# Optimization experiments

Hardware: AMD Instinct MI355X
Metric: run time of the kernel (lower is better)

## Reference

```python
import jax, jax.numpy as jnp
import numpy as np

NUM_HEADS = 16
NUM_KV_HEADS = 8
HEAD_DIM = 128
EPS = 1e-6
SLIDING_WINDOW = 1024
ROPE_THETA = 10000.0


def _rms_norm(x, w):
    # per-head RMSNorm in fp32, as in Qwen3RMSNorm
    xf = x.astype(jnp.float32)
    var = jnp.mean(xf * xf, axis=-1, keepdims=True)
    return (w * (xf * jax.lax.rsqrt(var + EPS))).astype(x.dtype)


def _rotate_half(x):
    d = x.shape[-1] // 2
    return jnp.concatenate([-x[..., d:], x[..., :d]], axis=-1)


def setup_inputs() -> dict:
    key = jax.random.key(0)
    ks = jax.random.split(key, 6)
    B, S, H = 2, 2048, 2048
    hidden_states = jax.random.normal(ks[0], (B, S, H), dtype=jnp.float32)
    # RoPE tables per HF convention: cos/sin of shape [B, S, head_dim]
    inv_freq = 1.0 / (ROPE_THETA ** (np.arange(0, HEAD_DIM, 2, dtype=np.float32) / HEAD_DIM))
    pos = np.arange(S, dtype=np.float32)
    ang = np.outer(pos, inv_freq)  # [S, HEAD_DIM/2]
    emb = np.concatenate([ang, ang], axis=-1)  # [S, HEAD_DIM]
    cos = jnp.broadcast_to(jnp.asarray(np.cos(emb)), (B, S, HEAD_DIM))
    sin = jnp.broadcast_to(jnp.asarray(np.sin(emb)), (B, S, HEAD_DIM))
    sc = 0.02
    Wq = jax.random.normal(ks[1], (NUM_HEADS * HEAD_DIM, H), dtype=jnp.float32) * sc
    Wk = jax.random.normal(ks[2], (NUM_KV_HEADS * HEAD_DIM, H), dtype=jnp.float32) * sc
    Wv = jax.random.normal(ks[3], (NUM_KV_HEADS * HEAD_DIM, H), dtype=jnp.float32) * sc
    Wo = jax.random.normal(ks[4], (H, NUM_HEADS * HEAD_DIM), dtype=jnp.float32) * sc
    q_norm_w = jnp.ones((HEAD_DIM,), dtype=jnp.float32)
    k_norm_w = jnp.ones((HEAD_DIM,), dtype=jnp.float32)
    return {"hidden_states": hidden_states, "cos": cos, "sin": sin,
            "Wq": Wq, "Wk": Wk, "Wv": Wv, "Wo": Wo,
            "q_norm_w": q_norm_w, "k_norm_w": k_norm_w}


def reference(hidden_states, cos, sin, Wq, Wk, Wv, Wo, q_norm_w, k_norm_w):
    B, S, H = hidden_states.shape
    scaling = HEAD_DIM ** -0.5
    # projections (torch Linear: y = x @ W.T), reshape to [B, nH, S, D]
    q = jnp.einsum('bsh,oh->bso', hidden_states, Wq).reshape(B, S, NUM_HEADS, HEAD_DIM)
    k = jnp.einsum('bsh,oh->bso', hidden_states, Wk).reshape(B, S, NUM_KV_HEADS, HEAD_DIM)
    v = jnp.einsum('bsh,oh->bso', hidden_states, Wv).reshape(B, S, NUM_KV_HEADS, HEAD_DIM)
    q = _rms_norm(q, q_norm_w).transpose(0, 2, 1, 3)  # [B, nH, S, D]
    k = _rms_norm(k, k_norm_w).transpose(0, 2, 1, 3)  # [B, nKV, S, D]
    v = v.transpose(0, 2, 1, 3)
    # RoPE, cos/sin broadcast over heads (unsqueeze_dim=1)
    c = cos[:, None, :, :]
    s = sin[:, None, :, :]
    q = q * c + _rotate_half(q) * s
    k = k * c + _rotate_half(k) * s
    # GQA: repeat kv heads
    groups = NUM_HEADS // NUM_KV_HEADS
    k = jnp.repeat(k, groups, axis=1)
    v = jnp.repeat(v, groups, axis=1)
    # causal + sliding-window mask
    i = jnp.arange(S)[:, None]
    j = jnp.arange(S)[None, :]
    mask = (j <= i) & (i - j < SLIDING_WINDOW)  # [S, S]
    scores = jnp.einsum('bhqd,bhkd->bhqk', q, k) * scaling
    scores = jnp.where(mask[None, None], scores, jnp.finfo(scores.dtype).min)
    probs = jax.nn.softmax(scores, axis=-1)
    attn = jnp.einsum('bhqk,bhkd->bhqd', probs, v)  # [B, nH, S, D]
    attn = attn.transpose(0, 2, 1, 3).reshape(B, S, NUM_HEADS * HEAD_DIM)
    out = jnp.einsum('bso,ho->bsh', attn, Wo)
    return out
```

## Files before the change

kernel.cpp:

```cpp
#include <hip/hip_runtime.h>
#include <stdint.h>

#define S_LEN 2048
#define BATCH 2
#define HID 2048
#define NH 16
#define NKV 8
#define HD 128
#define WINDOW 1024
#define SCALE 0.08838834764831845f
#define QKVW 4096

typedef unsigned short u16;
typedef unsigned int u32;
typedef __attribute__((ext_vector_type(8))) short short8;
typedef __attribute__((ext_vector_type(4))) float f32x4;
typedef __attribute__((ext_vector_type(16))) float f32x16;
typedef __attribute__((ext_vector_type(4))) u16 u16x4;

__device__ __forceinline__ u16 f2b(float f) {
  u32 u = __builtin_bit_cast(u32, f);
  return (u16)((u + 0x7fffu + ((u >> 16) & 1u)) >> 16);
}
__device__ __forceinline__ float b2f(u16 h) {
  u32 u = ((u32)h) << 16;
  return __builtin_bit_cast(float, u);
}
__device__ __forceinline__ u32 pk_bf16(float a, float b) {
  u32 d;
  asm("v_cvt_pk_bf16_f32 %0, %1, %2" : "=v"(d) : "v"(a), "v"(b));
  return d;
}

__device__ __forceinline__ void gload_lds16(const u16* g, u16* l) {
  __builtin_amdgcn_global_load_lds(
      (const __attribute__((address_space(1))) u32*)g,
      (__attribute__((address_space(3))) u32*)l, 16, 0, 0);
}

template <int N>
__device__ __forceinline__ void wait_vm() {
  if constexpr (N == 0) asm volatile("s_waitcnt vmcnt(0)" ::: "memory");
}

#define CQ0 2097152
#define CQ1 3145728
#define CQ2 3670016
#define CQ3 4194304
#define CQ4 5242880
__global__ __launch_bounds__(256) void k_conv5(const float* __restrict__ s0,
                                               const float* __restrict__ s1,
                                               const float* __restrict__ s2,
                                               const float* __restrict__ s3,
                                               const float* __restrict__ s4,
                                               u16* __restrict__ dst) {
  int i = blockIdx.x * blockDim.x + threadIdx.x;
  const int st = gridDim.x * blockDim.x;
  for (; i < CQ4; i += st) {
    const f32x4* src;
    if (i < CQ0)      src = (const f32x4*)s0 + i;
    else if (i < CQ1) src = (const f32x4*)s1 + (i - CQ0);
    else if (i < CQ2) src = (const f32x4*)s2 + (i - CQ1);
    else if (i < CQ3) src = (const f32x4*)s3 + (i - CQ2);
    else              src = (const f32x4*)s4 + (i - CQ3);
    f32x4 v = *src;
    u16x4 o;
    o[0] = f2b(v[0]); o[1] = f2b(v[1]); o[2] = f2b(v[2]); o[3] = f2b(v[3]);
    ((u16x4*)dst)[i] = o;
  }
}

__device__ __forceinline__ void store_c(u16* C, long idx, float v) { C[idx] = f2b(v); }
__device__ __forceinline__ void store_c(float* C, long idx, float v) { C[idx] = v; }

template <typename OutT>
__global__ __launch_bounds__(256, 4) void k_gemmS(const u16* __restrict__ A,
                                                  const u16* __restrict__ B,
                                                  OutT* __restrict__ C,
                                                  int M, int N, int K) {
  __shared__ u16 sA[128 * 64];
  __shared__ u16 sB[128 * 64];
  const int tid = threadIdx.x;
  const int lane = tid & 63;
  const int w = tid >> 6;
  const int l15 = lane & 15;
  const int lg = lane >> 4;
  const int wm = w >> 1;
  const int wn = w & 1;
  const int sw = l15 & 7;

  const int gx = gridDim.x;
  const int nwg = gx * gridDim.y;
  const int flat = blockIdx.y * gx + blockIdx.x;
  const int tile = (flat & 7) * (nwg >> 3) + (flat >> 3);
  const long m0 = (long)(tile / gx) * 128;
  const long n0 = (long)(tile % gx) * 128;

  const u16* Abase = A + m0 * K;
  const u16* Bbase = B + n0 * K;

  int aOff[4], bOff[4], dstOff[4];
#pragma unroll
  for (int i = 0; i < 4; ++i) {
    const int c = tid + i * 256;
    const int row = c >> 3, chs = c & 7;
    const int scol = (chs ^ (row & 7)) * 8;
    aOff[i] = row * K + scol;
    bOff[i] = row * K + scol;
    dstOff[i] = c * 8;
  }

  f32x4 acc[4][4];
  const f32x4 z4 = {0.f, 0.f, 0.f, 0.f};
#pragma unroll
  for (int i = 0; i < 4; ++i)
#pragma unroll
    for (int j = 0; j < 4; ++j) acc[i][j] = z4;

  const int arow = (wm * 64 + l15) * 64;
  const int brow = (wn * 64 + l15) * 64;
  const int akc0 = (lg ^ sw) * 8;
  const int akc1 = ((4 + lg) ^ sw) * 8;

  const int NT = K >> 6;

  for (int t = 0; t < NT; ++t) {
#pragma unroll
    for (int i = 0; i < 4; ++i)
      gload_lds16(Abase + aOff[i] + t * 64, &sA[dstOff[i]]);
#pragma unroll
    for (int i = 0; i < 4; ++i)
      gload_lds16(Bbase + bOff[i] + t * 64, &sB[dstOff[i]]);
    wait_vm<0>();
    __builtin_amdgcn_sched_barrier(0);
    __builtin_amdgcn_s_barrier();
    __builtin_amdgcn_sched_barrier(0);

#pragma unroll
    for (int kk = 0; kk < 2; ++kk) {
      const int akc = (kk == 0) ? akc0 : akc1;
      short8 afk[4], bfk[4];
#pragma unroll
      for (int i = 0; i < 4; ++i)
        afk[i] = *(const short8*)&sA[arow + i * 16 * 64 + akc];
#pragma unroll
      for (int j = 0; j < 4; ++j)
        bfk[j] = *(const short8*)&sB[brow + j * 16 * 64 + akc];
      __builtin_amdgcn_s_setprio(1);
#pragma unroll
      for (int i = 0; i < 4; ++i)
#pragma unroll
        for (int j = 0; j < 4; ++j)
          acc[i][j] = __builtin_amdgcn_mfma_f32_16x16x32_bf16(
              afk[i], bfk[j], acc[i][j], 0, 0, 0);
      __builtin_amdgcn_s_setprio(0);
    }
    __builtin_amdgcn_s_barrier();
    __builtin_amdgcn_sched_barrier(0);
  }

#pragma unroll
  for (int i = 0; i < 4; ++i)
#pragma unroll
    for (int j = 0; j < 4; ++j)
#pragma unroll
      for (int r = 0; r < 4; ++r) {
        long row = m0 + wm * 64 + i * 16 + lg * 4 + r;
        long col = n0 + wn * 64 + j * 16 + l15;
        store_c(C, row * (long)N + col, acc[i][j][r]);
      }
}

__global__ __launch_bounds__(256) void k_normrope(u16* __restrict__ QKV,
                                                  const float* __restrict__ cosb,
                                                  const float* __restrict__ sinb,
                                                  const float* __restrict__ qw,
                                                  const float* __restrict__ kw) {
  const int lane = threadIdx.x & 63;
  const int w = threadIdx.x >> 6;
  int row = blockIdx.x * 4 + w;
  const int nQ = BATCH * S_LEN * NH;
  u16* p;
  const float* nw;
  int tok;
  float sc;
  if (row < nQ) {
    tok = row >> 4;
    int h = row & 15;
    p = QKV + (long)tok * QKVW + h * HD;
    nw = qw;
    sc = SCALE;
  } else {
    int r2 = row - nQ;
    tok = r2 >> 3;
    int h = r2 & 7;
    p = QKV + (long)tok * QKVW + 2048 + h * HD;
    nw = kw;
    sc = 1.0f;
  }
  float x0 = b2f(p[lane]);
  float x1 = b2f(p[lane + 64]);
  float ss = x0 * x0 + x1 * x1;
#pragma unroll
  for (int mk = 1; mk < 64; mk <<= 1) ss += __shfl_xor(ss, mk, 64);
  float rinv = rsqrtf(ss * (1.0f / 128.0f) + 1e-6f);
  float y0 = x0 * rinv * nw[lane];
  float y1 = x1 * rinv * nw[lane + 64];
  const float* cp = cosb + (long)tok * HD;
  const float* sp = sinb + (long)tok * HD;
  float o0 = (y0 * cp[lane] - y1 * sp[lane]) * sc;
  float o1 = (y1 * cp[lane + 64] + y0 * sp[lane + 64]) * sc;
  p[lane] = f2b(o0);
  p[lane + 64] = f2b(o1);
}

__global__ __launch_bounds__(256, 2) void k_attn(const u16* __restrict__ QKV,
                                                 u16* __restrict__ AO) {
  __shared__ u16 sK[64 * 128];
  __shared__ u16 sVT[64 * 128];
  const int tid = threadIdx.x;
  const int lane = tid & 63;
  const int l31 = lane & 31;
  const int hi = lane >> 5;
  const int w = tid >> 6;
  const int q0 = blockIdx.x * 128;
  const int h = blockIdx.y;
  const int b = blockIdx.z;
  const int kvh = h >> 1;
  const int qw0 = q0 + w * 32;
  const int iq = qw0 + l31;

  const long tokbase = (long)b * S_LEN;
  const u16* Qrow = QKV + (tokbase + qw0 + l31) * QKVW + h * HD;
  short8 qf[8];
#pragma unroll
  for (int dt = 0; dt < 8; ++dt) qf[dt] = *(const short8*)(Qrow + dt * 16 + hi * 8);

  f32x16 o[4];
#pragma unroll
  for (int n = 0; n < 4; ++n)
#pragma unroll
    for (int r = 0; r < 16; ++r) o[n][r] = 0.f;
  float m = 0.f, lsum = 0.f;

  const u16* Kbase = QKV + tokbase * QKVW + 2048 + kvh * HD;
  const u16* Vbase = QKV + tokbase * QKVW + 3072 + kvh * HD;

  int kc_row[4], kc_off[4];
  u16* kc_dst[4];
#pragma unroll
  for (int i = 0; i < 4; ++i) {
    const int c = tid + 256 * i;
    kc_row[i] = c >> 4;
    kc_off[i] = (((c & 15) ^ ((c >> 4) & 7))) * 8;
    kc_dst[i] = &sK[c * 8];
  }
  const int rp = tid & 31;
  const int dc0 = tid >> 5;
  const int rg_st = rp >> 2;

  int t_lo = q0 - (WINDOW - 1);
  t_lo = (t_lo < 0 ? 0 : t_lo) >> 6;
  const int t_hi = (q0 + 127) >> 6;

  for (int t = t_lo; t <= t_hi; ++t) {
    const int kv0 = t << 6;
#pragma unroll
    for (int i = 0; i < 4; ++i)
      gload_lds16(Kbase + (long)(kv0 + kc_row[i]) * QKVW + kc_off[i], kc_dst[i]);
#pragma unroll
    for (int i = 0; i < 2; ++i) {
      const int dc = dc0 + i * 8;
      const u16* vp = Vbase + (long)(kv0 + 2 * rp) * QKVW + dc * 8;
      short8 v0 = *(const short8*)vp;
      short8 v1 = *(const short8*)(vp + QKVW);
#pragma unroll
      for (int e = 0; e < 8; ++e) {
        const int d = dc * 8 + e;
        const int unit = d * 8 + (rg_st ^ (d & 7));
        ((u32*)sVT)[unit * 4 + (rp & 3)] = (u32)(u16)v0[e] | ((u32)(u16)v1[e] << 16);
      }
    }
    __syncthreads();

    const bool skipw = (kv0 > qw0 + 31) || (kv0 + 63 < qw0 - (WINDOW - 1));
    if (!skipw) {
      const bool full = (kv0 + 63 <= qw0) && ((qw0 + 31) - kv0 < WINDOW);
      f32x16 s0, s1;
#pragma unroll
      for (int r = 0; r < 16; ++r) { s0[r] = 0.f; s1[r] = 0.f; }
      const int rsw = l31 & 7;
#pragma unroll
      for (int dt = 0; dt < 8; ++dt) {
        const int ch = hi + 2 * dt;
        const short8 kf0 = *(const short8*)&sK[(l31 * 16 + (ch ^ rsw)) * 8];
        s0 = __builtin_amdgcn_mfma_f32_32x32x16_bf16(kf0, qf[dt], s0, 0, 0, 0);
        const short8 kf1 = *(const short8*)&sK[((l31 + 32) * 16 + (ch ^ rsw)) * 8];
        s1 = __builtin_amdgcn_mfma_f32_32x32x16_bf16(kf1, qf[dt], s1, 0, 0, 0);
      }
      float p[32];
#pragma unroll
      for (int r = 0; r < 16; ++r) { p[r] = s0[r]; p[16 + r] = s1[r]; }
      if (!full) {
#pragma unroll
        for (int r = 0; r < 32; ++r) {
          const int kk = kv0 + (r >> 4) * 32 + 4 * hi + (r & 3) + 8 * ((r >> 2) & 3);
          p[r] = ((u32)(iq - kk) < (u32)WINDOW) ? p[r] : -3.0e38f;
        }
      }
      float tm = p[0];
#pragma unroll
      for (int r = 1; r < 32; ++r) tm = fmaxf(tm, p[r]);
      tm = fmaxf(tm, __shfl_xor(tm, 32, 64));
      const float mn = fmaxf(m, tm);
      const float al = __expf(m - mn);
      m = mn;
      float rs = 0.f;
#pragma unroll
      for (int r = 0; r < 32; ++r) { p[r] = __expf(p[r] - mn); rs += p[r]; }
      rs += __shfl_xor(rs, 32, 64);
      lsum = lsum * al + rs;
#pragma unroll
      for (int n = 0; n < 4; ++n)
#pragma unroll
        for (int r = 0; r < 16; ++r) o[n][r] *= al;

      short8 pf[4];
#pragma unroll
      for (int ks = 0; ks < 4; ++ks) {
        const int bb = (ks >> 1) * 16 + (ks & 1) * 8;
        u32 a0 = pk_bf16(p[bb + 0], p[bb + 1]);
        u32 b0 = pk_bf16(p[bb + 4], p[bb + 5]);
        u32 a1 = pk_bf16(p[bb + 2], p[bb + 3]);
        u32 b1 = pk_bf16(p[bb + 6], p[bb + 7]);
        asm volatile("v_permlane32_swap_b32 %0, %1" : "+v"(a0), "+v"(b0));
        asm volatile("v_permlane32_swap_b32 %0, %1" : "+v"(a1), "+v"(b1));
        union { u32 u[4]; short8 s; } uu;
        uu.u[0] = a0; uu.u[1] = a1; uu.u[2] = b0; uu.u[3] = b1;
        pf[ks] = uu.s;
      }
#pragma unroll
      for (int dt = 0; dt < 4; ++dt) {
        const int d = l31 + 32 * dt;
        const int dsw = d & 7;
#pragma unroll
        for (int ks = 0; ks < 4; ++ks) {
          const int rg = ks * 2 + hi;
          const short8 vf = *(const short8*)&sVT[(d * 8 + (rg ^ dsw)) * 8];
          o[dt] = __builtin_amdgcn_mfma_f32_32x32x16_bf16(vf, pf[ks], o[dt], 0, 0, 0);
        }
      }
    }
    __syncthreads();
  }

  __syncthreads();
  float* R = ((float*)sK) + w * 1024;
  const float rl = 1.0f / lsum;
  const int half = hi;
#pragma unroll
  for (int dt = 0; dt < 4; ++dt) {
#pragma unroll
    for (int r = 0; r < 16; ++r) {
      const int dp = 4 * hi + (r & 3) + 8 * (r >> 2);
      R[dp * 32 + (l31 ^ (4 * (dp & 7)))] = o[dt][r] * rl;
    }
    __syncthreads();
    union { u16 hh[16]; short8 s[2]; } U;
#pragma unroll
    for (int j = 0; j < 16; ++j) {
      const int dp = half * 16 + j;
      U.hh[j] = f2b(R[dp * 32 + (l31 ^ (4 * (dp & 7)))]);
    }
    u16* dst = AO + (tokbase + q0 + w * 32 + l31) * (NH * HD) + h * HD + dt * 32 + half * 16;
    *(short8*)dst = U.s[0];
    *(short8*)(dst + 8) = U.s[1];
    __syncthreads();
  }
}

extern "C" void kernel_launch(void* const* d_in, const int* in_sizes, int n_in,
                              void* d_out, int out_size, void* d_ws, size_t ws_size,
                              hipStream_t stream) {
  const float* hs   = (const float*)d_in[0];
  const float* cosb = (const float*)d_in[1];
  const float* sinb = (const float*)d_in[2];
  const float* Wq   = (const float*)d_in[3];
  const float* Wk   = (const float*)d_in[4];
  const float* Wv   = (const float*)d_in[5];
  const float* Wo   = (const float*)d_in[6];
  const float* qw   = (const float*)d_in[7];
  const float* kw   = (const float*)d_in[8];
  float* out = (float*)d_out;

  const long SZ_X  = (long)BATCH * S_LEN * HID;
  const long SZ_WQ = (long)NH * HD * HID;
  const long SZ_WK = (long)NKV * HD * HID;
  u16* Xb   = (u16*)d_ws;
  u16* Wqb  = Xb + SZ_X;
  u16* Wkb  = Wqb + SZ_WQ;
  u16* Wvb  = Wkb + SZ_WK;
  u16* Wob  = Wvb + SZ_WK;
  u16* QKVb = Wob + SZ_WQ;
  u16* AOb  = QKVb + (long)BATCH * S_LEN * QKVW;

  k_conv5<<<2048, 256, 0, stream>>>(hs, Wq, Wk, Wv, Wo, Xb);

  k_gemmS<u16><<<dim3(32, 32), 256, 0, stream>>>(
      Xb, Wqb, QKVb, BATCH * S_LEN, QKVW, HID);

  k_normrope<<<(BATCH * S_LEN * (NH + NKV)) / 4, 256, 0, stream>>>(QKVb, cosb, sinb, qw, kw);

  k_attn<<<dim3(S_LEN / 128, NH, BATCH), 256, 0, stream>>>(QKVb, AOb);

  k_gemmS<float><<<dim3(16, 32), 256, 0, stream>>>(
      AOb, Wob, out, BATCH * S_LEN, HID, HID);
}
```

Baseline: 209.0 us.

## Use 2-wave 128x128 GEMM variant with larger per-wave tiles for QKV projection

Adds a k_gemmV kernel that computes the same 128x128 output tile with 128 threads (2 waves) instead of 256, each wave covering all 128 rows by 64 columns with an 8x4 MFMA accumulator grid. The QKV projection GEMM launch switches to this kernel. The aim is more MFMA work per LDS fragment load and fewer waves sharing each barrier. In exchange, register pressure roughly doubles and occupancy drops (launch bounds of 2 blocks), with fewer waves available to hide load latency. The shared A/B offset array in k_gemmS is a minor cleanup.

```diff
diff --git a/kernel.cpp b/kernel.cpp
--- a/kernel.cpp
+++ b/kernel.cpp
@@ -74,6 +74,99 @@
 __device__ __forceinline__ void store_c(float* C, long idx, float v) { C[idx] = v; }
 
 template <typename OutT>
+__global__ __launch_bounds__(128, 2) void k_gemmV(const u16* __restrict__ A,
+                                                  const u16* __restrict__ B,
+                                                  OutT* __restrict__ C,
+                                                  int M, int N, int K) {
+  __shared__ u16 sA[128 * 64];
+  __shared__ u16 sB[128 * 64];
+  const int tid = threadIdx.x;
+  const int lane = tid & 63;
+  const int w = tid >> 6;
+  const int l15 = lane & 15;
+  const int lg = lane >> 4;
+  const int sw = l15 & 7;
+
+  const int gx = gridDim.x;
+  const int nwg = gx * gridDim.y;
+  const int flat = blockIdx.y * gx + blockIdx.x;
+  const int tile = (flat & 7) * (nwg >> 3) + (flat >> 3);
+  const long m0 = (long)(tile / gx) * 128;
+  const long n0 = (long)(tile % gx) * 128;
+
+  const u16* Abase = A + m0 * K;
+  const u16* Bbase = B + n0 * K;
+
+  int aOff[8], dstOff[8];
+#pragma unroll
+  for (int i = 0; i < 8; ++i) {
+    const int c = tid + i * 128;
+    const int row = c >> 3, chs = c & 7;
+    aOff[i] = row * K + (chs ^ (row & 7)) * 8;
+    dstOff[i] = c * 8;
+  }
+
+  f32x4 acc[8][4];
+  const f32x4 z4 = {0.f, 0.f, 0.f, 0.f};
+#pragma unroll
+  for (int i = 0; i < 8; ++i)
+#pragma unroll
+    for (int j = 0; j < 4; ++j) acc[i][j] = z4;
+
+  const int akc0 = (lg ^ sw) * 8;
+  const int akc1 = ((4 + lg) ^ sw) * 8;
+  const int brow0 = w * 64;
+
+  const int NT = K >> 6;
+
+  for (int t = 0; t < NT; ++t) {
+#pragma unroll
+    for (int i = 0; i < 8; ++i)
+      gload_lds16(Abase + aOff[i] + t * 64, &sA[dstOff[i]]);
+#pragma unroll
+    for (int i = 0; i < 8; ++i)
+      gload_lds16(Bbase + aOff[i] + t * 64, &sB[dstOff[i]]);
+    wait_vm<0>();
+    __builtin_amdgcn_sched_barrier(0);
+    __builtin_amdgcn_s_barrier();
+    __builtin_amdgcn_sched_barrier(0);
+
+#pragma unroll
+    for (int kk = 0; kk < 2; ++kk) {
+      const int akc = (kk == 0) ? akc0 : akc1;
+      short8 afk[8], bfk[4];
+#pragma unroll
+      for (int i = 0; i < 8; ++i)
+        afk[i] = *(const short8*)&sA[(i * 16 + l15) * 64 + akc];
+#pragma unroll
+      for (int j = 0; j < 4; ++j)
+        bfk[j] = *(const short8*)&sB[(brow0 + j * 16 + l15) * 64 + akc];
+      __builtin_amdgcn_s_setprio(1);
+#pragma unroll
+      for (int i = 0; i < 8; ++i)
+#pragma unroll
+        for (int j = 0; j < 4; ++j)
+          acc[i][j] = __builtin_amdgcn_mfma_f32_16x16x32_bf16(
+              afk[i], bfk[j], acc[i][j], 0, 0, 0);
+      __builtin_amdgcn_s_setprio(0);
+    }
+    __builtin_amdgcn_s_barrier();
+    __builtin_amdgcn_sched_barrier(0);
+  }
+
+#pragma unroll
+  for (int i = 0; i < 8; ++i)
+#pragma unroll
+    for (int j = 0; j < 4; ++j)
+#pragma unroll
+      for (int r = 0; r < 4; ++r) {
+        long row = m0 + i * 16 + lg * 4 + r;
+        long col = n0 + w * 64 + j * 16 + l15;
+        store_c(C, row * (long)N + col, acc[i][j][r]);
+      }
+}
+
+template <typename OutT>
 __global__ __launch_bounds__(256, 4) void k_gemmS(const u16* __restrict__ A,
                                                   const u16* __restrict__ B,
                                                   OutT* __restrict__ C,
@@ -99,14 +192,12 @@
   const u16* Abase = A + m0 * K;
   const u16* Bbase = B + n0 * K;
 
-  int aOff[4], bOff[4], dstOff[4];
+  int aOff[4], dstOff[4];
 #pragma unroll
   for (int i = 0; i < 4; ++i) {
     const int c = tid + i * 256;
     const int row = c >> 3, chs = c & 7;
-    const int scol = (chs ^ (row & 7)) * 8;
-    aOff[i] = row * K + scol;
-    bOff[i] = row * K + scol;
+    aOff[i] = row * K + (chs ^ (row & 7)) * 8;
     dstOff[i] = c * 8;
   }
 
@@ -130,7 +221,7 @@
       gload_lds16(Abase + aOff[i] + t * 64, &sA[dstOff[i]]);
 #pragma unroll
     for (int i = 0; i < 4; ++i)
-      gload_lds16(Bbase + bOff[i] + t * 64, &sB[dstOff[i]]);
+      gload_lds16(Bbase + aOff[i] + t * 64, &sB[dstOff[i]]);
     wait_vm<0>();
     __builtin_amdgcn_sched_barrier(0);
     __builtin_amdgcn_s_barrier();
@@ -406,7 +497,7 @@
 
   k_conv5<<<2048, 256, 0, stream>>>(hs, Wq, Wk, Wv, Wo, Xb);
 
-  k_gemmS<u16><<<dim3(32, 32), 256, 0, stream>>>(
+  k_gemmV<u16><<<dim3(32, 32), 128, 0, stream>>>(
       Xb, Wqb, QKVb, BATCH * S_LEN, QKVW, HID);
 
   k_normrope<<<(BATCH * S_LEN * (NH + NKV)) / 4, 256, 0, stream>>>(QKVb, cosb, sinb, qw, kw);
```

Result: faster. 203.2 us (-2.8%).

## Fuse Q norm and RoPE into attention, add lazy softmax rescale

Applied to the files above, without the earlier changes.

Q-side RMSNorm, RoPE and scaling now run inside the attention kernel on the loaded Q fragments, so the separate norm kernel handles only K heads. This removes a read and write pass over Q. The online softmax now skips the max update and rescaling of the output accumulators unless the new tile max exceeds the running max by more than 8. The GEMM launch-bounds occupancy hint rises from 4 to 5, and the duplicate B offset array is dropped. The lazy rescale risks larger intermediate values, and the tighter register budget may cause spills in the GEMM.

```diff
diff --git a/kernel.cpp b/kernel.cpp
--- a/kernel.cpp
+++ b/kernel.cpp
@@ -74,7 +74,7 @@
 __device__ __forceinline__ void store_c(float* C, long idx, float v) { C[idx] = v; }
 
 template <typename OutT>
-__global__ __launch_bounds__(256, 4) void k_gemmS(const u16* __restrict__ A,
+__global__ __launch_bounds__(256, 5) void k_gemmS(const u16* __restrict__ A,
                                                   const u16* __restrict__ B,
                                                   OutT* __restrict__ C,
                                                   int M, int N, int K) {
@@ -99,14 +99,12 @@
   const u16* Abase = A + m0 * K;
   const u16* Bbase = B + n0 * K;
 
-  int aOff[4], bOff[4], dstOff[4];
+  int aOff[4], dstOff[4];
 #pragma unroll
   for (int i = 0; i < 4; ++i) {
     const int c = tid + i * 256;
     const int row = c >> 3, chs = c & 7;
-    const int scol = (chs ^ (row & 7)) * 8;
-    aOff[i] = row * K + scol;
-    bOff[i] = row * K + scol;
+    aOff[i] = row * K + (chs ^ (row & 7)) * 8;
     dstOff[i] = c * 8;
   }
 
@@ -130,7 +128,7 @@
       gload_lds16(Abase + aOff[i] + t * 64, &sA[dstOff[i]]);
 #pragma unroll
     for (int i = 0; i < 4; ++i)
-      gload_lds16(Bbase + bOff[i] + t * 64, &sB[dstOff[i]]);
+      gload_lds16(Bbase + aOff[i] + t * 64, &sB[dstOff[i]]);
     wait_vm<0>();
     __builtin_amdgcn_sched_barrier(0);
     __builtin_amdgcn_s_barrier();
@@ -171,51 +169,35 @@
       }
 }
 
-__global__ __launch_bounds__(256) void k_normrope(u16* __restrict__ QKV,
-                                                  const float* __restrict__ cosb,
-                                                  const float* __restrict__ sinb,
-                                                  const float* __restrict__ qw,
-                                                  const float* __restrict__ kw) {
+__global__ __launch_bounds__(256) void k_normropeK(u16* __restrict__ QKV,
+                                                   const float* __restrict__ cosb,
+                                                   const float* __restrict__ sinb,
+                                                   const float* __restrict__ kw) {
   const int lane = threadIdx.x & 63;
   const int w = threadIdx.x >> 6;
-  int row = blockIdx.x * 4 + w;
-  const int nQ = BATCH * S_LEN * NH;
-  u16* p;
-  const float* nw;
-  int tok;
-  float sc;
-  if (row < nQ) {
-    tok = row >> 4;
-    int h = row & 15;
-    p = QKV + (long)tok * QKVW + h * HD;
-    nw = qw;
-    sc = SCALE;
-  } else {
-    int r2 = row - nQ;
-    tok = r2 >> 3;
-    int h = r2 & 7;
-    p = QKV + (long)tok * QKVW + 2048 + h * HD;
-    nw = kw;
-    sc = 1.0f;
-  }
+  const int row = blockIdx.x * 4 + w;
+  const int tok = row >> 3;
+  const int h = row & 7;
+  u16* p = QKV + (long)tok * QKVW + 2048 + h * HD;
   float x0 = b2f(p[lane]);
   float x1 = b2f(p[lane + 64]);
   float ss = x0 * x0 + x1 * x1;
 #pragma unroll
   for (int mk = 1; mk < 64; mk <<= 1) ss += __shfl_xor(ss, mk, 64);
   float rinv = rsqrtf(ss * (1.0f / 128.0f) + 1e-6f);
-  float y0 = x0 * rinv * nw[lane];
-  float y1 = x1 * rinv * nw[lane + 64];
+  float y0 = x0 * rinv * kw[lane];
+  float y1 = x1 * rinv * kw[lane + 64];
   const float* cp = cosb + (long)tok * HD;
   const float* sp = sinb + (long)tok * HD;
-  float o0 = (y0 * cp[lane] - y1 * sp[lane]) * sc;
-  float o1 = (y1 * cp[lane + 64] + y0 * sp[lane + 64]) * sc;
-  p[lane] = f2b(o0);
-  p[lane + 64] = f2b(o1);
+  p[lane] = f2b(y0 * cp[lane] - y1 * sp[lane]);
+  p[lane + 64] = f2b(y1 * cp[lane + 64] + y0 * sp[lane + 64]);
 }
 
 __global__ __launch_bounds__(256, 2) void k_attn(const u16* __restrict__ QKV,
-                                                 u16* __restrict__ AO) {
+                                                 u16* __restrict__ AO,
+                                                 const float* __restrict__ qwp,
+                                                 const float* __restrict__ cosb,
+                                                 const float* __restrict__ sinb) {
   __shared__ u16 sK[64 * 128];
   __shared__ u16 sVT[64 * 128];
   const int tid = threadIdx.x;
@@ -231,10 +213,39 @@
   const int iq = qw0 + l31;
 
   const long tokbase = (long)b * S_LEN;
-  const u16* Qrow = QKV + (tokbase + qw0 + l31) * QKVW + h * HD;
+  const long gtok = tokbase + qw0 + l31;
+  const u16* Qrow = QKV + gtok * QKVW + h * HD;
   short8 qf[8];
 #pragma unroll
   for (int dt = 0; dt < 8; ++dt) qf[dt] = *(const short8*)(Qrow + dt * 16 + hi * 8);
+  {
+    float ss = 0.f;
+#pragma unroll
+    for (int dt = 0; dt < 8; ++dt)
+#pragma unroll
+      for (int j = 0; j < 8; ++j) {
+        const float f = b2f((u16)qf[dt][j]);
+        ss += f * f;
+      }
+    ss += __shfl_xor(ss, 32, 64);
+    const float rinv = rsqrtf(ss * (1.0f / 128.0f) + 1e-6f);
+    const float* cp = cosb + gtok * HD;
+    const float* sp = sinb + gtok * HD;
+#pragma unroll
+    for (int dt = 0; dt < 4; ++dt) {
+      const int d0 = dt * 16 + hi * 8;
+#pragma unroll
+      for (int j = 0; j < 8; ++j) {
+        const int d = d0 + j;
+        const float y0 = b2f((u16)qf[dt][j]) * rinv * qwp[d];
+        const float y1 = b2f((u16)qf[dt + 4][j]) * rinv * qwp[d + 64];
+        const float o0 = (y0 * cp[d] - y1 * sp[d]) * SCALE;
+        const float o1 = (y1 * cp[d + 64] + y0 * sp[d + 64]) * SCALE;
+        qf[dt][j] = (short)f2b(o0);
+        qf[dt + 4][j] = (short)f2b(o1);
+      }
+    }
+  }
 
   f32x16 o[4];
 #pragma unroll
@@ -312,18 +323,21 @@
 #pragma unroll
       for (int r = 1; r < 32; ++r) tm = fmaxf(tm, p[r]);
       tm = fmaxf(tm, __shfl_xor(tm, 32, 64));
-      const float mn = fmaxf(m, tm);
-      const float al = __expf(m - mn);
-      m = mn;
+      if (!__all(tm - m <= 8.0f)) {
+        const float mn = fmaxf(m, tm);
+        const float al = __expf(m - mn);
+        m = mn;
+        lsum *= al;
+#pragma unroll
+        for (int n = 0; n < 4; ++n)
+#pragma unroll
+          for (int r = 0; r < 16; ++r) o[n][r] *= al;
+      }
       float rs = 0.f;
 #pragma unroll
-      for (int r = 0; r < 32; ++r) { p[r] = __expf(p[r] - mn); rs += p[r]; }
+      for (int r = 0; r < 32; ++r) { p[r] = __expf(p[r] - m); rs += p[r]; }
       rs += __shfl_xor(rs, 32, 64);
-      lsum = lsum * al + rs;
-#pragma unroll
-      for (int n = 0; n < 4; ++n)
-#pragma unroll
-        for (int r = 0; r < 16; ++r) o[n][r] *= al;
+      lsum += rs;
 
       short8 pf[4];
 #pragma unroll
@@ -409,9 +423,9 @@
   k_gemmS<u16><<<dim3(32, 32), 256, 0, stream>>>(
       Xb, Wqb, QKVb, BATCH * S_LEN, QKVW, HID);
 
-  k_normrope<<<(BATCH * S_LEN * (NH + NKV)) / 4, 256, 0, stream>>>(QKVb, cosb, sinb, qw, kw);
-
-  k_attn<<<dim3(S_LEN / 128, NH, BATCH), 256, 0, stream>>>(QKVb, AOb);
+  k_normropeK<<<(BATCH * S_LEN * NKV) / 4, 256, 0, stream>>>(QKVb, cosb, sinb, kw);
+
+  k_attn<<<dim3(S_LEN / 128, NH, BATCH), 256, 0, stream>>>(QKVb, AOb, qw, cosb, sinb);
 
   k_gemmS<float><<<dim3(16, 32), 256, 0, stream>>>(
       AOb, Wob, out, BATCH * S_LEN, HID, HID);
```

Measured after the change: 473.0 us. +126.3%, slower.

## Share K/V tiles across GQA head pair in one 512-thread attention block

Applied to the files above, without the earlier changes.

The attention kernel now launches one 512-thread block per KV head instead of one 256-thread block per query head. Both query heads of a GQA group use the same K and V tiles staged in LDS, which halves global K/V loads and LDS staging work per query head. It also adds a lazy online-softmax rescale: the running max and the output accumulators are rescaled only when some lane's new max exceeds the old by more than 8. Larger blocks can lower occupancy and raise barrier cost, and skipping the rescale lets exponentials reach up to e^8 before normalization.

```diff
diff --git a/kernel.cpp b/kernel.cpp
--- a/kernel.cpp
+++ b/kernel.cpp
@@ -99,14 +99,12 @@
   const u16* Abase = A + m0 * K;
   const u16* Bbase = B + n0 * K;
 
-  int aOff[4], bOff[4], dstOff[4];
+  int aOff[4], dstOff[4];
 #pragma unroll
   for (int i = 0; i < 4; ++i) {
     const int c = tid + i * 256;
     const int row = c >> 3, chs = c & 7;
-    const int scol = (chs ^ (row & 7)) * 8;
-    aOff[i] = row * K + scol;
-    bOff[i] = row * K + scol;
+    aOff[i] = row * K + (chs ^ (row & 7)) * 8;
     dstOff[i] = c * 8;
   }
 
@@ -130,7 +128,7 @@
       gload_lds16(Abase + aOff[i] + t * 64, &sA[dstOff[i]]);
 #pragma unroll
     for (int i = 0; i < 4; ++i)
-      gload_lds16(Bbase + bOff[i] + t * 64, &sB[dstOff[i]]);
+      gload_lds16(Bbase + aOff[i] + t * 64, &sB[dstOff[i]]);
     wait_vm<0>();
     __builtin_amdgcn_sched_barrier(0);
     __builtin_amdgcn_s_barrier();
@@ -214,20 +212,21 @@
   p[lane + 64] = f2b(o1);
 }
 
-__global__ __launch_bounds__(256, 2) void k_attn(const u16* __restrict__ QKV,
+__global__ __launch_bounds__(512, 2) void k_attn(const u16* __restrict__ QKV,
                                                  u16* __restrict__ AO) {
-  __shared__ u16 sK[64 * 128];
-  __shared__ u16 sVT[64 * 128];
+  __shared__ u16 smem[2 * 64 * 128];
+  u16* const sK = smem;
+  u16* const sVT = smem + 64 * 128;
   const int tid = threadIdx.x;
   const int lane = tid & 63;
   const int l31 = lane & 31;
   const int hi = lane >> 5;
   const int w = tid >> 6;
   const int q0 = blockIdx.x * 128;
-  const int h = blockIdx.y;
+  const int kvh = blockIdx.y;
   const int b = blockIdx.z;
-  const int kvh = h >> 1;
-  const int qw0 = q0 + w * 32;
+  const int h = kvh * 2 + (w >> 2);
+  const int qw0 = q0 + (w & 3) * 32;
   const int iq = qw0 + l31;
 
   const long tokbase = (long)b * S_LEN;
@@ -246,17 +245,17 @@
   const u16* Kbase = QKV + tokbase * QKVW + 2048 + kvh * HD;
   const u16* Vbase = QKV + tokbase * QKVW + 3072 + kvh * HD;
 
-  int kc_row[4], kc_off[4];
-  u16* kc_dst[4];
-#pragma unroll
-  for (int i = 0; i < 4; ++i) {
-    const int c = tid + 256 * i;
+  int kc_row[2], kc_off[2];
+  u16* kc_dst[2];
+#pragma unroll
+  for (int i = 0; i < 2; ++i) {
+    const int c = tid + 512 * i;
     kc_row[i] = c >> 4;
     kc_off[i] = (((c & 15) ^ ((c >> 4) & 7))) * 8;
     kc_dst[i] = &sK[c * 8];
   }
   const int rp = tid & 31;
-  const int dc0 = tid >> 5;
+  const int dc = tid >> 5;
   const int rg_st = rp >> 2;
 
   int t_lo = q0 - (WINDOW - 1);
@@ -266,11 +265,9 @@
   for (int t = t_lo; t <= t_hi; ++t) {
     const int kv0 = t << 6;
 #pragma unroll
-    for (int i = 0; i < 4; ++i)
+    for (int i = 0; i < 2; ++i)
       gload_lds16(Kbase + (long)(kv0 + kc_row[i]) * QKVW + kc_off[i], kc_dst[i]);
-#pragma unroll
-    for (int i = 0; i < 2; ++i) {
-      const int dc = dc0 + i * 8;
+    {
       const u16* vp = Vbase + (long)(kv0 + 2 * rp) * QKVW + dc * 8;
       short8 v0 = *(const short8*)vp;
       short8 v1 = *(const short8*)(vp + QKVW);
@@ -312,18 +309,21 @@
 #pragma unroll
       for (int r = 1; r < 32; ++r) tm = fmaxf(tm, p[r]);
       tm = fmaxf(tm, __shfl_xor(tm, 32, 64));
-      const float mn = fmaxf(m, tm);
-      const float al = __expf(m - mn);
-      m = mn;
+      if (!__all(tm - m <= 8.0f)) {
+        const float mn = fmaxf(m, tm);
+        const float al = __expf(m - mn);
+        m = mn;
+        lsum *= al;
+#pragma unroll
+        for (int n = 0; n < 4; ++n)
+#pragma unroll
+          for (int r = 0; r < 16; ++r) o[n][r] *= al;
+      }
       float rs = 0.f;
 #pragma unroll
-      for (int r = 0; r < 32; ++r) { p[r] = __expf(p[r] - mn); rs += p[r]; }
+      for (int r = 0; r < 32; ++r) { p[r] = __expf(p[r] - m); rs += p[r]; }
       rs += __shfl_xor(rs, 32, 64);
-      lsum = lsum * al + rs;
-#pragma unroll
-      for (int n = 0; n < 4; ++n)
-#pragma unroll
-        for (int r = 0; r < 16; ++r) o[n][r] *= al;
+      lsum += rs;
 
       short8 pf[4];
 #pragma unroll
@@ -355,7 +355,7 @@
   }
 
   __syncthreads();
-  float* R = ((float*)sK) + w * 1024;
+  float* R = ((float*)smem) + w * 1024;
   const float rl = 1.0f / lsum;
   const int half = hi;
 #pragma unroll
@@ -372,7 +372,7 @@
       const int dp = half * 16 + j;
       U.hh[j] = f2b(R[dp * 32 + (l31 ^ (4 * (dp & 7)))]);
     }
-    u16* dst = AO + (tokbase + q0 + w * 32 + l31) * (NH * HD) + h * HD + dt * 32 + half * 16;
+    u16* dst = AO + (tokbase + qw0 + l31) * (NH * HD) + h * HD + dt * 32 + half * 16;
     *(short8*)dst = U.s[0];
     *(short8*)(dst + 8) = U.s[1];
     __syncthreads();
@@ -409,9 +409,10 @@
   k_gemmS<u16><<<dim3(32, 32), 256, 0, stream>>>(
       Xb, Wqb, QKVb, BATCH * S_LEN, QKVW, HID);
 
-  k_normrope<<<(BATCH * S_LEN * (NH + NKV)) / 4, 256, 0, stream>>>(QKVb, cosb, sinb, qw, kw);
-
-  k_attn<<<dim3(S_LEN / 128, NH, BATCH), 256, 0, stream>>>(QKVb, AOb);
+  k_normrope<<<(BATCH * S_LEN * (NH + NKV)) / 4, 256, 0, stream>>>(
+      QKVb, cosb, sinb, qw, kw);
+
+  k_attn<<<dim3(S_LEN / 128, NKV, BATCH), 512, 0, stream>>>(QKVb, AOb);
 
   k_gemmS<float><<<dim3(16, 32), 256, 0, stream>>>(
       AOb, Wob, out, BATCH * S_LEN, HID, HID);
```

Measured after the change: 209.8 us. No clear change (+0.4%).
